# Optimization experiments

Hardware: AMD Instinct MI355X
Metric: run time of the kernel (lower is better)

The kernel has to match this reference:

```python
import jax, jax.numpy as jnp
import numpy as np
from jax import lax

E = 20          # num experts / classes
BN_EPS = 1e-5


def _conv(x, w, b=None):
    # NCHW conv, stride 1, 'same' padding (kernel 3x3 or 1x1)
    y = lax.conv_general_dilated(x, w, (1, 1), 'SAME',
                                 dimension_numbers=('NCHW', 'OIHW', 'NCHW'))
    return y if b is None else y + b[None, :, None, None]


def _lrelu(x):
    return jnp.where(x >= 0, x, 0.2 * x)


def _bn(x, g, b, m, v):
    # inference-mode batchnorm
    scale = g * lax.rsqrt(v + BN_EPS)
    return x * scale[None, :, None, None] + (b - m * scale)[None, :, None, None]


def setup_inputs() -> dict:
    key = jax.random.key(0)
    ks = iter(jax.random.split(key, 40))
    def w(shape):
        return jax.random.normal(next(ks), shape, jnp.float32) * 0.05
    d = {}
    d['x'] = jax.random.normal(next(ks), (2, 3, 192, 192), jnp.float32)
    d['noise'] = jax.random.normal(next(ks), (2, 128, 192, 192), jnp.float32)
    # classification head
    d['cls_w1'] = w((64, 3, 3, 3));    d['cls_b1'] = jnp.zeros((64,), jnp.float32)
    d['cls_w2'] = w((128, 64, 3, 3));  d['cls_b2'] = jnp.zeros((128,), jnp.float32)
    d['cls_w3'] = w((256, 128, 3, 3)); d['cls_b3'] = jnp.zeros((256,), jnp.float32)
    d['cls_w4'] = w((512, 256, 1, 1)); d['cls_b4'] = jnp.zeros((512,), jnp.float32)
    d['cls_w5'] = w((E, 512, 1, 1));   d['cls_b5'] = jnp.zeros((E,), jnp.float32)
    for c, i in ((128, 1), (256, 2), (512, 3)):
        d[f'bn{i}_g'] = jnp.ones((c,), jnp.float32)
        d[f'bn{i}_b'] = jnp.zeros((c,), jnp.float32)
        d[f'bn{i}_m'] = jnp.zeros((c,), jnp.float32)
        d[f'bn{i}_v'] = jnp.ones((c,), jnp.float32)
    # 20 expert encoders (stacked on leading axis)
    d['enc_w1'] = w((E, 32, 3, 3, 3));    d['enc_b1'] = jnp.zeros((E, 32), jnp.float32)
    d['enc_w2'] = w((E, 64, 32, 3, 3));   d['enc_b2'] = jnp.zeros((E, 64), jnp.float32)
    d['enc_w3'] = w((E, 128, 64, 3, 3));  d['enc_b3'] = jnp.zeros((E, 128), jnp.float32)
    d['enc_w4'] = w((E, 128, 128, 3, 3)); d['enc_b4'] = jnp.zeros((E, 128), jnp.float32)
    # decoder (legacy=False: first two 1x1 convs have no bias)
    d['dec_w1'] = w((64, 128, 1, 1))
    d['dec_w2'] = w((32, 64, 1, 1))
    d['dec_w3'] = w((3, 32, 1, 1)); d['dec_b3'] = jnp.zeros((3,), jnp.float32)
    return d


def reference(x, noise,
              cls_w1, cls_b1, cls_w2, cls_b2, cls_w3, cls_b3,
              cls_w4, cls_b4, cls_w5, cls_b5,
              bn1_g, bn1_b, bn1_m, bn1_v,
              bn2_g, bn2_b, bn2_m, bn2_v,
              bn3_g, bn3_b, bn3_m, bn3_v,
              enc_w1, enc_b1, enc_w2, enc_b2, enc_w3, enc_b3, enc_w4, enc_b4,
              dec_w1, dec_w2, dec_w3, dec_b3):
    B, _, H, W = x.shape
    C = enc_w4.shape[1]  # 128
    # --- classification / routing ---
    h = _lrelu(_conv(x, cls_w1, cls_b1))
    h = _lrelu(_bn(_conv(h, cls_w2, cls_b2), bn1_g, bn1_b, bn1_m, bn1_v))
    h = _lrelu(_bn(_conv(h, cls_w3, cls_b3), bn2_g, bn2_b, bn2_m, bn2_v))
    h = _lrelu(_bn(_conv(h, cls_w4, cls_b4), bn3_g, bn3_b, bn3_m, bn3_v))
    classes = jax.nn.softmax(_conv(h, cls_w5, cls_b5), axis=1)  # [B,E,H,W]
    idx = jnp.argmax(classes, axis=1)  # [B,H,W] top-1 expert per pixel

    # --- run all 20 dense encoders (faithful to original torch.where masking) ---
    def enc(w1, b1, w2, b2, w3, b3, w4, b4):
        e = _lrelu(_conv(x, w1, b1))
        e = _lrelu(_conv(e, w2, b2))
        e = _lrelu(_conv(e, w3, b3))
        return _conv(e, w4, b4)
    embs = jax.vmap(enc)(enc_w1, enc_b1, enc_w2, enc_b2,
                         enc_w3, enc_b3, enc_w4, enc_b4)  # [E,B,128,H,W]
    embs = jnp.moveaxis(embs, 0, 1)  # [B,E,128,H,W]
    sel_idx = jnp.broadcast_to(idx[:, None, None, :, :], (B, 1, C, H, W))
    emb = jnp.take_along_axis(embs, sel_idx, axis=1)[:, 0]  # [B,128,H,W]

    # --- decode with additive noise ---
    d = _conv(emb + noise, dec_w1)
    d = _conv(d, dec_w2)
    out = _conv(d, dec_w3, dec_b3)  # [B,3,H,W]

    # --- load balancing loss ---
    one_hot = jax.nn.one_hot(idx, E, dtype=jnp.float32)          # [B,H,W,E]
    density = one_hot.reshape(B, -1, E).mean(axis=1)             # [B,E]
    density_proxy = classes.reshape(B, E, -1).mean(axis=-1)      # [B,E]
    lb = (density_proxy * density).mean() * float(E * E)
    return out, lb * 0.1
```

## Files before the change

kernel.cpp:

```cpp
#include <hip/hip_runtime.h>
#include <hip/hip_bf16.h>

typedef __hip_bfloat16 bf16;
typedef unsigned short u16;
typedef short s16x8 __attribute__((ext_vector_type(8)));
typedef float f32x4 __attribute__((ext_vector_type(4)));
#define MFMA16(a, b, c) __builtin_amdgcn_mfma_f32_16x16x32_bf16(a, b, c, 0, 0, 0)

#define HW_   36864
#define WP_   194
#define HWP_  37636
#define W_    192
#define SP_   9216

__device__ __forceinline__ float ldin(const void* p, size_t i, int f32) {
    return f32 ? ((const float*)p)[i] : __bfloat162float(((const bf16*)p)[i]);
}
__device__ __forceinline__ int probe_f32(const void* pr) {
    return ((const unsigned*)pr)[0] == 0x3F800000u;
}
__device__ __forceinline__ u16 f2bf(float f) {
    bf16 h = __float2bfloat16(f);
    return *reinterpret_cast<u16*>(&h);
}

__global__ __launch_bounds__(256) void pad_x_k(const void* __restrict__ x,
                                               float* __restrict__ xpad,
                                               const void* __restrict__ pr) {
    const int f32 = probe_f32(pr);
    int i = blockIdx.x * 256 + threadIdx.x;
    if (i >= 2 * 3 * HW_) return;
    int w = i % W_;
    int h = (i / W_) % W_;
    int c = i / HW_;
    xpad[(size_t)c * HWP_ + (size_t)(h + 1) * WP_ + (w + 1)] = ldin(x, i, f32);
}

__global__ __launch_bounds__(256) void conv3x3_k(
    const float* __restrict__ in, const void* __restrict__ wgt,
    const void* __restrict__ bias, const void* __restrict__ bng,
    const void* __restrict__ bnb, const void* __restrict__ bnm,
    const void* __restrict__ bnv, float* __restrict__ out,
    int Cin, int Cout, int lrelu, const void* __restrict__ pr)
{
    extern __shared__ float wl[];
    const int f32 = probe_f32(pr);
    const int tid = threadIdx.x;
    const int co0 = blockIdx.y * 8;
    const int b   = blockIdx.z;
    const int n = Cin * 72;
    for (int i = tid; i < n; i += 256) {
        int u = i & 7, r = i >> 3;
        int ci = r / 9, tap = r - ci * 9;
        wl[i] = ldin(wgt, ((size_t)(co0 + u) * Cin + ci) * 9 + tap, f32);
    }
    __syncthreads();

    const int pixb = blockIdx.x * 1024 + tid;
    int off[4];
#pragma unroll
    for (int p = 0; p < 4; ++p) {
        int pix = pixb + p * 256;
        int h = pix / W_, w = pix - h * W_;
        off[p] = (h + 1) * WP_ + (w + 1);
    }
    float acc[32];
#pragma unroll
    for (int i = 0; i < 32; ++i) acc[i] = 0.f;

    const int doff[9] = {-(WP_+1), -WP_, -(WP_-1), -1, 0, 1, WP_-1, WP_, WP_+1};
    const float* inb = in + (size_t)b * Cin * HWP_;
    for (int ci = 0; ci < Cin; ++ci) {
        const float* ip = inb + (size_t)ci * HWP_;
        const float* wp = wl + ci * 72;
#pragma unroll
        for (int tap = 0; tap < 9; ++tap) {
            const float4 wa = *(const float4*)(wp + tap * 8);
            const float4 wb = *(const float4*)(wp + tap * 8 + 4);
            const int d = doff[tap];
            float v[4];
#pragma unroll
            for (int p = 0; p < 4; ++p) v[p] = ip[off[p] + d];
#pragma unroll
            for (int p = 0; p < 4; ++p) {
                acc[p*8+0] += v[p] * wa.x;  acc[p*8+1] += v[p] * wa.y;
                acc[p*8+2] += v[p] * wa.z;  acc[p*8+3] += v[p] * wa.w;
                acc[p*8+4] += v[p] * wb.x;  acc[p*8+5] += v[p] * wb.y;
                acc[p*8+6] += v[p] * wb.z;  acc[p*8+7] += v[p] * wb.w;
            }
        }
    }

#pragma unroll
    for (int u = 0; u < 8; ++u) {
        const int co = co0 + u;
        float s = 1.f, t = 0.f;
        if (bng) {
            float g = ldin(bng, co, f32), bb = ldin(bnb, co, f32);
            float m = ldin(bnm, co, f32), vv = ldin(bnv, co, f32);
            s = g * rsqrtf(vv + 1e-5f);
            t = bb - m * s;
        }
        const float bs = bias ? ldin(bias, co, f32) : 0.f;
        float* op = out + ((size_t)b * Cout + co) * HWP_;
#pragma unroll
        for (int p = 0; p < 4; ++p) {
            float val = (acc[p*8+u] + bs) * s + t;
            if (lrelu) val = val >= 0.f ? val : 0.2f * val;
            op[off[p]] = val;
        }
    }
}

__global__ __launch_bounds__(256) void conv1x1s_k(
    const float* __restrict__ in, const void* __restrict__ wgt,
    const void* __restrict__ bias, const void* __restrict__ bng,
    const void* __restrict__ bnb, const void* __restrict__ bnm,
    const void* __restrict__ bnv, float* __restrict__ out,
    int Cin, int pix0, const void* __restrict__ pr)
{
    extern __shared__ float wl[];
    const int f32 = probe_f32(pr);
    const int tid = threadIdx.x;
    const int co0 = blockIdx.y * 8;
    const int b   = blockIdx.z;
    const int n = Cin * 8;
    for (int i = tid; i < n; i += 256) {
        int u = i & 7, ci = i >> 3;
        wl[i] = ldin(wgt, (size_t)(co0 + u) * Cin + ci, f32);
    }
    __syncthreads();

    const int pixb = pix0 + blockIdx.x * 1024 + tid;
    int off[4], lp[4];
#pragma unroll
    for (int p = 0; p < 4; ++p) {
        int pix = pixb + p * 256;
        lp[p] = pix - pix0;
        int h = pix / W_, w = pix - h * W_;
        off[p] = (h + 1) * WP_ + (w + 1);
    }
    float acc[32];
#pragma unroll
    for (int i = 0; i < 32; ++i) acc[i] = 0.f;

    for (int ci = 0; ci < Cin; ++ci) {
        const float* ip = in + ((size_t)b * Cin + ci) * HWP_;
        const float4 wa = *(const float4*)(wl + ci * 8);
        const float4 wb = *(const float4*)(wl + ci * 8 + 4);
        float v[4];
#pragma unroll
        for (int p = 0; p < 4; ++p) v[p] = ip[off[p]];
#pragma unroll
        for (int p = 0; p < 4; ++p) {
            acc[p*8+0] += v[p] * wa.x;  acc[p*8+1] += v[p] * wa.y;
            acc[p*8+2] += v[p] * wa.z;  acc[p*8+3] += v[p] * wa.w;
            acc[p*8+4] += v[p] * wb.x;  acc[p*8+5] += v[p] * wb.y;
            acc[p*8+6] += v[p] * wb.z;  acc[p*8+7] += v[p] * wb.w;
        }
    }

#pragma unroll
    for (int u = 0; u < 8; ++u) {
        const int co = co0 + u;
        float g = ldin(bng, co, f32), bb = ldin(bnb, co, f32);
        float m = ldin(bnm, co, f32), vv = ldin(bnv, co, f32);
        float s = g * rsqrtf(vv + 1e-5f);
        float t = bb - m * s;
        const float bs = ldin(bias, co, f32);
        float* op = out + ((size_t)b * 512 + co) * SP_;
#pragma unroll
        for (int p = 0; p < 4; ++p) {
            float val = (acc[p*8+u] + bs) * s + t;
            val = val >= 0.f ? val : 0.2f * val;
            op[lp[p]] = val;
        }
    }
}

__global__ __launch_bounds__(256) void heads_k(
    const float* __restrict__ c4q, const void* __restrict__ w5,
    const void* __restrict__ b5, int* __restrict__ idx,
    float* __restrict__ proxy, float* __restrict__ cntg, int pix0,
    const void* __restrict__ pr)
{
    extern __shared__ float wl[];
    __shared__ float sums[20];
    __shared__ float cnts[20];
    const int f32 = probe_f32(pr);
    const int tid = threadIdx.x;
    const int b = blockIdx.y;
    for (int i = tid; i < 512 * 20; i += 256) {
        int e = i % 20, ci = i / 20;
        wl[ci * 20 + e] = ldin(w5, (size_t)e * 512 + ci, f32);
    }
    if (tid < 20) { sums[tid] = 0.f; cnts[tid] = 0.f; }
    __syncthreads();

    const int lpix = blockIdx.x * 256 + tid;

    float acc[20];
#pragma unroll
    for (int e = 0; e < 20; ++e) acc[e] = ldin(b5, e, f32);
    const float* ip = c4q + (size_t)b * 512 * SP_;
    for (int ci = 0; ci < 512; ++ci) {
        const float v = ip[(size_t)ci * SP_ + lpix];
        const float* wp = wl + ci * 20;
#pragma unroll
        for (int e = 0; e < 20; ++e) acc[e] += v * wp[e];
    }

    float m = acc[0]; int am = 0;
#pragma unroll
    for (int e = 1; e < 20; ++e) if (acc[e] > m) { m = acc[e]; am = e; }
    float prb[20], ssum = 0.f;
#pragma unroll
    for (int e = 0; e < 20; ++e) { prb[e] = expf(acc[e] - m); ssum += prb[e]; }
    const float inv = 1.f / ssum;
    idx[b * HW_ + pix0 + lpix] = am;

    const int lane = tid & 63;
#pragma unroll
    for (int e = 0; e < 20; ++e) {
        float p = prb[e] * inv;
        p += __shfl_down(p, 32); p += __shfl_down(p, 16); p += __shfl_down(p, 8);
        p += __shfl_down(p, 4);  p += __shfl_down(p, 2);  p += __shfl_down(p, 1);
        if (lane == 0) atomicAdd(&sums[e], p);
        unsigned long long bal = __ballot(am == e);
        if (lane == 0) atomicAdd(&cnts[e], (float)__popcll(bal));
    }
    __syncthreads();
    if (tid < 20) {
        atomicAdd(&proxy[b * 20 + tid], sums[tid]);
        atomicAdd(&cntg[b * 20 + tid], cnts[tid]);
    }
}

__global__ __launch_bounds__(256) void wtx_k(const void* __restrict__ w,
                                             u16* __restrict__ wt,
                                             int Cout, int Cin, int nTot,
                                             const void* __restrict__ pr) {
    const int f32 = probe_f32(pr);
    int i = blockIdx.x * 256 + threadIdx.x;
    if (i >= nTot) return;
    int ci = i % Cin; int r = i / Cin;
    int co = r % Cout; r /= Cout;
    int tap = r % 9; int e = r / 9;
    size_t src = ((size_t)(e * Cout + co) * Cin + ci) * 9 + tap;
    wt[i] = f2bf(ldin(w, src, f32));
}

__global__ __launch_bounds__(512) void fused_expert_k(
    const float* __restrict__ xpad, const int* __restrict__ idx,
    const void* __restrict__ ew1, const void* __restrict__ eb1,
    const u16* __restrict__ Wt2, const void* __restrict__ eb2,
    const u16* __restrict__ Wt3, const void* __restrict__ eb3,
    const u16* __restrict__ Wt4, const void* __restrict__ eb4,
    float* __restrict__ emb, const void* __restrict__ pr)
{
    __shared__ __align__(16) char smem_[137216];
    u16*   e2s = (u16*)smem_;
    u16*   e3s = (u16*)(smem_ + 54272);
    u16*   e1s = (u16*)(smem_ + 54272);
    float* xs  = (float*)smem_;
    float* wl1 = (float*)(smem_ + 6912);
    u16*   w2s = (u16*)(smem_ + 86016);
    __shared__ int s_sel[256];
    __shared__ int s_wc[8];

    const int f32 = probe_f32(pr);
    const int tid  = threadIdx.x;
    const int lane = tid & 63, wv = tid >> 6;
    const int ml = lane & 15, q8 = (lane >> 4) * 8, m0 = (lane >> 4) * 4;
    const int b = blockIdx.y;
    const int eid = blockIdx.z;
    const int ty = blockIdx.x / 12, tx = blockIdx.x - ty * 12;
    const int Oh = ty * 16, Ow = tx * 16;

    {
        int sel = 0;
        if (tid < 256) {
            const int r = tid >> 4, c = tid & 15;
            sel = (idx[b * HW_ + (Oh + r) * W_ + (Ow + c)] == eid);
        }
        const unsigned long long m = __ballot(sel);
        if (lane == 0) s_wc[wv] = __popcll(m);
        __syncthreads();
        int cnt = 0;
#pragma unroll
        for (int w = 0; w < 8; ++w) cnt += s_wc[w];
        if (cnt == 0) return;
        int pre = 0;
        for (int w = 0; w < wv; ++w) pre += s_wc[w];
        if (sel)
            s_sel[pre + __popcll(m & ((1ull << lane) - 1ull))] = tid;
    }

    for (int i = tid; i < 24 * 24 * 3; i += 512) {
        int ch = i % 3, pxl = i / 3;
        int r = pxl / 24, c = pxl - r * 24;
        int ir = Oh - 4 + r, ic = Ow - 4 + c;
        float v = 0.f;
        if (ir >= -1 && ir < 193 && ic >= -1 && ic < 193)
            v = xpad[((size_t)b * 3 + ch) * HWP_ + (size_t)(ir + 1) * WP_ + (ic + 1)];
        xs[pxl * 3 + ch] = v;
    }
    for (int i = tid; i < 896; i += 512) {
        if (i < 864) {
            int co = i & 31, k = i >> 5;
            int ci = k / 9, tap = k - ci * 9;
            wl1[i] = ldin(ew1, (size_t)eid * 864 + ((size_t)co * 3 + ci) * 9 + tap, f32);
        } else {
            wl1[i] = ldin(eb1, (size_t)eid * 32 + (i - 864), f32);
        }
    }
    {
        const u16* Wt2e = Wt2 + (size_t)eid * 9 * 64 * 32;
        for (int i = tid; i < 2304; i += 512) {
            int r = i >> 2, part = i & 3;
            *(uint4*)(w2s + (size_t)r * 40 + part * 8) =
                *(const uint4*)(Wt2e + (size_t)r * 32 + part * 8);
        }
    }
    __syncthreads();

    if (tid < 484) {
        const int p = tid;
        const int r1 = p / 22, c1 = p - r1 * 22;
        const int ir = Oh - 3 + r1, ic = Ow - 3 + c1;
        const int inimg = (ir >= 0 && ir < 192 && ic >= 0 && ic < 192);
        float a1[32];
#pragma unroll
        for (int co = 0; co < 32; ++co) a1[co] = 0.f;
        if (inimg) {
#pragma unroll
            for (int ci = 0; ci < 3; ++ci)
#pragma unroll
                for (int tap = 0; tap < 9; ++tap) {
                    const int dy = tap / 3, dx = tap - dy * 3;
                    const float xv = xs[((r1 + dy) * 24 + (c1 + dx)) * 3 + ci];
                    const float* wp = wl1 + (ci * 9 + tap) * 32;
#pragma unroll
                    for (int co = 0; co < 32; ++co) a1[co] += xv * wp[co];
                }
        }
        u16 pk[32];
#pragma unroll
        for (int co = 0; co < 32; ++co) {
            float v = 0.f;
            if (inimg) {
                v = a1[co] + wl1[864 + co];
                v = v >= 0.f ? v : 0.2f * v;
            }
            pk[co] = f2bf(v);
        }
#pragma unroll
        for (int ch = 0; ch < 4; ++ch)
            *(uint4*)(e1s + ((size_t)ch * 488 + p) * 8) = ((const uint4*)pk)[ch];
    }
    __syncthreads();

    {
        int pxv[4], r2v[4], c2v[4];
#pragma unroll
        for (int j = 0; j < 4; ++j) {
            int t = wv + 8 * j; if (t > 24) t = 24;
            int px = t * 16 + ml;
            pxv[j] = px; r2v[j] = px / 20; c2v[j] = px - (px / 20) * 20;
        }
        f32x4 acc2[4][4];
#pragma unroll
        for (int j = 0; j < 4; ++j)
#pragma unroll
            for (int n = 0; n < 4; ++n) acc2[j][n] = (f32x4){0.f,0.f,0.f,0.f};

#pragma unroll
        for (int tap = 0; tap < 9; ++tap) {
            const int dy = tap / 3, dx = tap - dy * 3;
            s16x8 aW[4];
#pragma unroll
            for (int n = 0; n < 4; ++n)
                aW[n] = *(const s16x8*)(w2s + ((size_t)tap * 64 + n * 16 + ml) * 40 + q8);
#pragma unroll
            for (int j = 0; j < 4; ++j) {
                const int lin = (r2v[j] + dy) * 22 + (c2v[j] + dx);
                const s16x8 bA = *(const s16x8*)(e1s + ((size_t)(q8 >> 3) * 488 + lin) * 8);
#pragma unroll
                for (int n = 0; n < 4; ++n) acc2[j][n] = MFMA16(aW[n], bA, acc2[j][n]);
            }
        }
        __syncthreads();
#pragma unroll
        for (int j = 0; j < 4; ++j) {
            const int px = pxv[j];
            const int r2 = r2v[j], c2 = c2v[j];
            const int ir = Oh - 2 + r2, ic = Ow - 2 + c2;
            const int inimg = (ir >= 0 && ir < 192 && ic >= 0 && ic < 192);
#pragma unroll
            for (int n = 0; n < 4; ++n) {
                u16 pk[4];
#pragma unroll
                for (int r = 0; r < 4; ++r) {
                    const int co = n * 16 + m0 + r;
                    float v = 0.f;
                    if (inimg) {
                        v = acc2[j][n][r] + ldin(eb2, (size_t)eid * 64 + co, f32);
                        v = v >= 0.f ? v : 0.2f * v;
                    }
                    pk[r] = f2bf(v);
                }
                const int chunk = (n * 16 + m0) >> 3;
                *(uint2*)(e2s + ((size_t)chunk * 424 + px) * 8 + (m0 & 4)) = *(const uint2*)pk;
            }
        }
    }
    __syncthreads();

    {
        const u16* Wt3e = Wt3 + (size_t)eid * 9 * 128 * 64;
        const int np = wv >> 2;
        const int w4 = wv & 3;
        int pxv[6], r3v[6], c3v[6];
#pragma unroll
        for (int j = 0; j < 6; ++j) {
            int t = w4 + 4 * j; if (t > 20) t = 20;
            int px = t * 16 + ml;
            pxv[j] = px; r3v[j] = px / 18; c3v[j] = px - (px / 18) * 18;
        }
        f32x4 acc3[6][4];
#pragma unroll
        for (int j = 0; j < 6; ++j)
#pragma unroll
            for (int n = 0; n < 4; ++n) acc3[j][n] = (f32x4){0.f,0.f,0.f,0.f};

#pragma unroll
        for (int tap = 0; tap < 9; ++tap) {
            const int dy = tap / 3, dx = tap - dy * 3;
#pragma unroll
            for (int cc = 0; cc < 2; ++cc) {
                s16x8 aW[4];
#pragma unroll
                for (int n = 0; n < 4; ++n) {
                    const int co = np * 64 + n * 16 + ml;
                    aW[n] = *(const s16x8*)(Wt3e + ((size_t)tap * 128 + co) * 64 + cc * 32 + q8);
                }
                const int chunk = cc * 4 + (q8 >> 3);
#pragma unroll
                for (int j = 0; j < 6; ++j) {
                    const int lin = (r3v[j] + dy) * 20 + (c3v[j] + dx);
                    const s16x8 bA = *(const s16x8*)(e2s + ((size_t)chunk * 424 + lin) * 8);
#pragma unroll
                    for (int n = 0; n < 4; ++n) acc3[j][n] = MFMA16(aW[n], bA, acc3[j][n]);
                }
            }
        }
        float b3[4][4];
#pragma unroll
        for (int n = 0; n < 4; ++n)
#pragma unroll
            for (int r = 0; r < 4; ++r)
                b3[n][r] = ldin(eb3, (size_t)eid * 128 + np * 64 + n * 16 + m0 + r, f32);
#pragma unroll
        for (int j = 0; j < 6; ++j) {
            const int px = pxv[j];
            if (px >= 324) continue;
            const int r3 = r3v[j], c3 = c3v[j];
            const int ir = Oh - 1 + r3, ic = Ow - 1 + c3;
            const int inimg = (ir >= 0 && ir < 192 && ic >= 0 && ic < 192);
#pragma unroll
            for (int n = 0; n < 4; ++n) {
                u16 pk[4];
#pragma unroll
                for (int r = 0; r < 4; ++r) {
                    float v = 0.f;
                    if (inimg) {
                        v = acc3[j][n][r] + b3[n][r];
                        v = v >= 0.f ? v : 0.2f * v;
                    }
                    pk[r] = f2bf(v);
                }
                const int chunk = (np * 64 + n * 16 + m0) >> 3;
                *(uint2*)(e3s + ((size_t)chunk * 324 + px) * 8 + (m0 & 4)) = *(const uint2*)pk;
            }
        }
    }
    __syncthreads();

    {
        const u16* Wt4e = Wt4 + (size_t)eid * 9 * 128 * 128;
        int cnt = 0;
#pragma unroll
        for (int w = 0; w < 8; ++w) cnt += s_wc[w];
        const int mtiles = (cnt + 15) >> 4;
        const int n0 = wv * 16;
        float bs[4];
#pragma unroll
        for (int r = 0; r < 4; ++r) bs[r] = ldin(eb4, (size_t)eid * 128 + n0 + m0 + r, f32);
        for (int mt = 0; mt < mtiles; ++mt) {
            const int li = mt * 16 + ml;
            const int lpx = (li < cnt) ? s_sel[li] : 0;
            const int rr = lpx >> 4, cc2 = lpx & 15;
            f32x4 acc = {0.f,0.f,0.f,0.f};
#pragma unroll
            for (int tap = 0; tap < 9; ++tap) {
                const int dy = tap / 3, dx = tap - dy * 3;
                const int lin = (rr + dy) * 18 + (cc2 + dx);
#pragma unroll
                for (int c0 = 0; c0 < 128; c0 += 32) {
                    const s16x8 bA = *(const s16x8*)(e3s + ((size_t)((c0 + q8) >> 3) * 324 + lin) * 8);
                    const s16x8 aW = *(const s16x8*)(Wt4e + ((size_t)tap * 128 + n0 + ml) * 128 + c0 + q8);
                    acc = MFMA16(aW, bA, acc);
                }
            }
            if (li < cnt) {
                const int g = (Oh + rr) * W_ + Ow + cc2;
#pragma unroll
                for (int r = 0; r < 4; ++r)
                    emb[((size_t)b * 128 + n0 + m0 + r) * HW_ + g] = acc[r] + bs[r];
            }
        }
    }
}

__global__ __launch_bounds__(256) void dec_fused_k(
    const float* __restrict__ emb, const void* __restrict__ noise,
    const void* __restrict__ dw1, const void* __restrict__ dw2,
    const void* __restrict__ dw3, const void* __restrict__ db3,
    void* __restrict__ outb, const void* __restrict__ pr)
{
    __shared__ float w1s[128 * 64];
    __shared__ float w2s[64 * 32];
    __shared__ float w3s[100];
    const int f32 = probe_f32(pr);
    const int tid = threadIdx.x;
    for (int i = tid; i < 128 * 64; i += 256) {
        int ci = i >> 6, co = i & 63;
        w1s[i] = ldin(dw1, (size_t)co * 128 + ci, f32);
    }
    for (int i = tid; i < 64 * 32; i += 256) {
        int ci = i >> 5, co = i & 31;
        w2s[i] = ldin(dw2, (size_t)co * 64 + ci, f32);
    }
    if (tid < 96) {
        int ci = tid / 3, k = tid - ci * 3;
        w3s[ci * 3 + k] = ldin(dw3, (size_t)k * 32 + ci, f32);
    }
    if (tid >= 96 && tid < 99) w3s[96 + tid - 96] = ldin(db3, tid - 96, f32);
    __syncthreads();

    const int b = blockIdx.y;
    const int pix = blockIdx.x * 256 + tid;

    float h1[64];
#pragma unroll
    for (int i = 0; i < 64; ++i) h1[i] = 0.f;
    for (int ci = 0; ci < 128; ++ci) {
        const size_t base = ((size_t)b * 128 + ci) * HW_ + pix;
        const float v = emb[base] + ldin(noise, base, f32);
        const float* wp = w1s + ci * 64;
#pragma unroll
        for (int c4 = 0; c4 < 16; ++c4) {
            const float4 w = *(const float4*)(wp + c4 * 4);
            h1[c4*4+0] += v * w.x; h1[c4*4+1] += v * w.y;
            h1[c4*4+2] += v * w.z; h1[c4*4+3] += v * w.w;
        }
    }
    float h2[32];
#pragma unroll
    for (int i = 0; i < 32; ++i) h2[i] = 0.f;
#pragma unroll
    for (int ci = 0; ci < 64; ++ci) {
        const float v = h1[ci];
        const float* wp = w2s + ci * 32;
#pragma unroll
        for (int c4 = 0; c4 < 8; ++c4) {
            const float4 w = *(const float4*)(wp + c4 * 4);
            h2[c4*4+0] += v * w.x; h2[c4*4+1] += v * w.y;
            h2[c4*4+2] += v * w.z; h2[c4*4+3] += v * w.w;
        }
    }
    float a0 = w3s[96], a1 = w3s[97], a2 = w3s[98];
#pragma unroll
    for (int ci = 0; ci < 32; ++ci) {
        const float v = h2[ci];
        a0 += v * w3s[ci * 3 + 0];
        a1 += v * w3s[ci * 3 + 1];
        a2 += v * w3s[ci * 3 + 2];
    }
    const size_t o0 = (size_t)(b * 3 + 0) * HW_ + pix;
    const size_t o1 = (size_t)(b * 3 + 1) * HW_ + pix;
    const size_t o2 = (size_t)(b * 3 + 2) * HW_ + pix;
    if (f32) {
        ((float*)outb)[o0] = a0; ((float*)outb)[o1] = a1; ((float*)outb)[o2] = a2;
    } else {
        ((bf16*)outb)[o0] = __float2bfloat16(a0);
        ((bf16*)outb)[o1] = __float2bfloat16(a1);
        ((bf16*)outb)[o2] = __float2bfloat16(a2);
    }
}

__global__ void lb_k(const float* __restrict__ proxy, const float* __restrict__ cnt,
                     void* __restrict__ out, const void* __restrict__ pr) {
    const int f32 = probe_f32(pr);
    const int t = threadIdx.x;
    const float inv = 1.0f / (float)HW_;
    float v = 0.f;
    if (t < 40) v = (proxy[t] * inv) * (cnt[t] * inv);
#pragma unroll
    for (int o = 32; o > 0; o >>= 1) v += __shfl_down(v, o);
    if (t == 0) {
        if (f32) ((float*)out)[221184] = v;
        else     ((bf16*)out)[221184] = __float2bfloat16(v);
    }
}

extern "C" void kernel_launch(void* const* d_in, const int* in_sizes, int n_in,
                              void* d_out, int out_size, void* d_ws, size_t ws_size,
                              hipStream_t stream) {
    (void)in_sizes; (void)n_in; (void)out_size; (void)ws_size;
    const void* x    = d_in[0];
    const void* noise= d_in[1];
    const void* cw1  = d_in[2];  const void* cb1 = d_in[3];
    const void* cw2  = d_in[4];  const void* cb2 = d_in[5];
    const void* cw3  = d_in[6];  const void* cb3 = d_in[7];
    const void* cw4  = d_in[8];  const void* cb4 = d_in[9];
    const void* cw5  = d_in[10]; const void* cb5 = d_in[11];
    const void* bn1g = d_in[12]; const void* bn1b = d_in[13];
    const void* bn1m = d_in[14]; const void* bn1v = d_in[15];
    const void* bn2g = d_in[16]; const void* bn2b = d_in[17];
    const void* bn2m = d_in[18]; const void* bn2v = d_in[19];
    const void* bn3g = d_in[20]; const void* bn3b = d_in[21];
    const void* bn3m = d_in[22]; const void* bn3v = d_in[23];
    const void* ew1  = d_in[24]; const void* eb1 = d_in[25];
    const void* ew2  = d_in[26]; const void* eb2 = d_in[27];
    const void* ew3  = d_in[28]; const void* eb3 = d_in[29];
    const void* ew4  = d_in[30]; const void* eb4 = d_in[31];
    const void* dw1  = d_in[32];
    const void* dw2  = d_in[33];
    const void* dw3  = d_in[34]; const void* db3 = d_in[35];
    const void* pr   = bn1v;

    char* ws = (char*)d_ws;
    constexpr size_t SZ_XPAD = (((size_t)2*3*HWP_*4) + 255) & ~(size_t)255;
    constexpr size_t O_BUF2  = SZ_XPAD;
    constexpr size_t SZ_BUF2 = (size_t)2*256*HWP_*4;
    constexpr size_t O_BUF1  = O_BUF2 + SZ_BUF2;
    constexpr size_t SZ_BUF1 = (size_t)2*128*HWP_*4;
    constexpr size_t O_IDX   = O_BUF1 + SZ_BUF1;
    constexpr size_t O_STAT  = O_IDX + (size_t)2*HW_*4;
    constexpr size_t WS_USED = O_STAT + 512;

    float* xpad  = (float*)(ws);
    float* buf2  = (float*)(ws + O_BUF2);
    int*   idx   = (int*)  (ws + O_IDX);
    float* proxy = (float*)(ws + O_STAT);
    float* cntg  = proxy + 40;

    float* c1  = buf2;
    float* c3  = buf2;
    float* c2  = (float*)(ws + O_BUF1);
    float* c4q = (float*)(ws + O_BUF1);
    float* emb = buf2;
    u16* Wt2 = (u16*)(ws + O_BUF1);
    u16* Wt3 = Wt2 + 368640;
    u16* Wt4 = Wt3 + 1474560;

    hipMemsetAsync(d_ws, 0, WS_USED, stream);

    dim3 blk(256);
    pad_x_k<<<dim3((2*3*HW_ + 255)/256), blk, 0, stream>>>(x, xpad, pr);

    conv3x3_k<<<dim3(36,  8, 2), blk,   3*288, stream>>>(xpad, cw1, cb1, nullptr,nullptr,nullptr,nullptr, c1,   3,  64, 1, pr);
    conv3x3_k<<<dim3(36, 16, 2), blk,  64*288, stream>>>(c1,   cw2, cb2, bn1g,bn1b,bn1m,bn1v,           c2,  64, 128, 1, pr);
    conv3x3_k<<<dim3(36, 32, 2), blk, 128*288, stream>>>(c2,   cw3, cb3, bn2g,bn2b,bn2m,bn2v,           c3, 128, 256, 1, pr);
    for (int s = 0; s < 4; ++s) {
        conv1x1s_k<<<dim3(9, 64, 2), blk, 256*32, stream>>>(c3, cw4, cb4, bn3g,bn3b,bn3m,bn3v, c4q, 256, s*SP_, pr);
        heads_k<<<dim3(36, 2), blk, 512*20*4, stream>>>(c4q, cw5, cb5, idx, proxy, cntg, s*SP_, pr);
    }

    wtx_k<<<dim3(1440),  blk, 0, stream>>>(ew2, Wt2,  64,  32,  368640, pr);
    wtx_k<<<dim3(5760),  blk, 0, stream>>>(ew3, Wt3, 128,  64, 1474560, pr);
    wtx_k<<<dim3(11520), blk, 0, stream>>>(ew4, Wt4, 128, 128, 2949120, pr);

    fused_expert_k<<<dim3(144, 2, 20), dim3(512), 0, stream>>>(
        xpad, idx, ew1, eb1, Wt2, eb2, Wt3, eb3, Wt4, eb4, emb, pr);

    dec_fused_k<<<dim3(144, 2), blk, 0, stream>>>(emb, noise, dw1, dw2, dw3, db3, d_out, pr);
    lb_k<<<1, 64, 0, stream>>>(proxy, cntg, d_out, pr);
}
```

Measured before the change: 2.507 ms.

## Compact conv3 to pixels needed by selected outputs and software-pipeline weight loads

Builds a compacted list of the 18x18 layer-3 pixels that are actually needed by the selected output pixels (dilated selection mask), and computes conv3 only for those tiles instead of all 324 positions. Conv3 and conv4 weight loads are double-buffered so global weight fetches overlap MFMA work. Conv4 now processes up to four 16-pixel tiles per weight fetch, reusing each weight fragment across more pixels. This adds per-block scan overhead and extra register pressure from the multi-buffered fragments and accumulators.

Result: no change. 2.508 ms (+0.1%).

```diff
diff --git a/kernel.cpp b/kernel.cpp
--- a/kernel.cpp
+++ b/kernel.cpp
@@ -267,6 +267,9 @@
     u16*   w2s = (u16*)(smem_ + 86016);
     __shared__ int s_sel[256];
     __shared__ int s_wc[8];
+    __shared__ unsigned long long s_selq[4];
+    __shared__ u16 s_l3[324];
+    __shared__ int s_c3;
 
     const int f32 = probe_f32(pr);
     const int tid  = threadIdx.x;
@@ -284,7 +287,10 @@
             sel = (idx[b * HW_ + (Oh + r) * W_ + (Ow + c)] == eid);
         }
         const unsigned long long m = __ballot(sel);
-        if (lane == 0) s_wc[wv] = __popcll(m);
+        if (lane == 0) {
+            s_wc[wv] = __popcll(m);
+            if (wv < 4) s_selq[wv] = m;
+        }
         __syncthreads();
         int cnt = 0;
 #pragma unroll
@@ -294,6 +300,36 @@
         for (int w = 0; w < wv; ++w) pre += s_wc[w];
         if (sel)
             s_sel[pre + __popcll(m & ((1ull << lane) - 1ull))] = tid;
+    }
+
+    if (wv == 0) {
+        unsigned need = 0;
+        const int r3 = lane;
+        if (r3 < 18) {
+            unsigned m = 0;
+#pragma unroll
+            for (int d = 0; d < 3; ++d) {
+                const int r = r3 - 2 + d;
+                if (r >= 0 && r < 16)
+                    m |= (unsigned)((s_selq[r >> 2] >> ((r & 3) * 16)) & 0xFFFFull);
+            }
+            need = (m | (m << 1) | (m << 2)) & 0x3FFFFu;
+        }
+        const int pc = __popc(need);
+        int inc = pc;
+#pragma unroll
+        for (int o = 1; o < 32; o <<= 1) {
+            const int t = __shfl_up(inc, o);
+            if (lane >= o) inc += t;
+        }
+        int k = inc - pc;
+        unsigned mm = need;
+        while (mm) {
+            const int c = __ffs(mm) - 1;
+            mm &= mm - 1;
+            s_l3[k++] = (u16)(r3 * 18 + c);
+        }
+        if (lane == 17) s_c3 = inc;
     }
 
     for (int i = tid; i < 24 * 24 * 3; i += 512) {
@@ -420,11 +456,15 @@
         const u16* Wt3e = Wt3 + (size_t)eid * 9 * 128 * 64;
         const int np = wv >> 2;
         const int w4 = wv & 3;
+        const int cnt3 = s_c3;
+        const int tiles3 = (cnt3 + 15) >> 4;
+        const int jc = (w4 < tiles3) ? ((tiles3 - w4 + 3) >> 2) : 0;
         int pxv[6], r3v[6], c3v[6];
 #pragma unroll
         for (int j = 0; j < 6; ++j) {
-            int t = w4 + 4 * j; if (t > 20) t = 20;
-            int px = t * 16 + ml;
+            int li = (w4 + 4 * j) * 16 + ml;
+            if (li >= cnt3) li = cnt3 - 1;
+            const int px = s_l3[li];
             pxv[j] = px; r3v[j] = px / 18; c3v[j] = px - (px / 18) * 18;
         }
         f32x4 acc3[6][4];
@@ -433,27 +473,35 @@
 #pragma unroll
             for (int n = 0; n < 4; ++n) acc3[j][n] = (f32x4){0.f,0.f,0.f,0.f};
 
-#pragma unroll
-        for (int tap = 0; tap < 9; ++tap) {
-            const int dy = tap / 3, dx = tap - dy * 3;
-#pragma unroll
-            for (int cc = 0; cc < 2; ++cc) {
-                s16x8 aW[4];
-#pragma unroll
-                for (int n = 0; n < 4; ++n) {
-                    const int co = np * 64 + n * 16 + ml;
-                    aW[n] = *(const s16x8*)(Wt3e + ((size_t)tap * 128 + co) * 64 + cc * 32 + q8);
-                }
-                const int chunk = cc * 4 + (q8 >> 3);
-#pragma unroll
-                for (int j = 0; j < 6; ++j) {
-                    const int lin = (r3v[j] + dy) * 20 + (c3v[j] + dx);
-                    const s16x8 bA = *(const s16x8*)(e2s + ((size_t)chunk * 424 + lin) * 8);
-#pragma unroll
-                    for (int n = 0; n < 4; ++n) acc3[j][n] = MFMA16(aW[n], bA, acc3[j][n]);
-                }
-            }
-        }
+#define LW3(dst, g) { const int tp_ = (g) >> 1, cc_ = (g) & 1;                         \
+    dst[0] = *(const s16x8*)(Wt3e + ((size_t)tp_*128 + np*64 +  0 + ml)*64 + cc_*32 + q8); \
+    dst[1] = *(const s16x8*)(Wt3e + ((size_t)tp_*128 + np*64 + 16 + ml)*64 + cc_*32 + q8); \
+    dst[2] = *(const s16x8*)(Wt3e + ((size_t)tp_*128 + np*64 + 32 + ml)*64 + cc_*32 + q8); \
+    dst[3] = *(const s16x8*)(Wt3e + ((size_t)tp_*128 + np*64 + 48 + ml)*64 + cc_*32 + q8); }
+#define C3GROUP(BUF, g) { const int tp_ = (g) >> 1, cc_ = (g) & 1;                     \
+    const int dy_ = tp_ / 3, dx_ = tp_ - dy_ * 3;                                      \
+    const int ch_ = cc_ * 4 + (q8 >> 3);                                               \
+    _Pragma("unroll")                                                                  \
+    for (int j = 0; j < 6; ++j) if (j < jc) {                                          \
+        const int lin_ = (r3v[j] + dy_) * 20 + (c3v[j] + dx_);                         \
+        const s16x8 bA_ = *(const s16x8*)(e2s + ((size_t)ch_ * 424 + lin_) * 8);       \
+        acc3[j][0] = MFMA16(BUF[0], bA_, acc3[j][0]);                                  \
+        acc3[j][1] = MFMA16(BUF[1], bA_, acc3[j][1]);                                  \
+        acc3[j][2] = MFMA16(BUF[2], bA_, acc3[j][2]);                                  \
+        acc3[j][3] = MFMA16(BUF[3], bA_, acc3[j][3]); } }
+
+        s16x8 aA[4], aB[4];
+        LW3(aA, 0);
+#pragma unroll
+        for (int g = 0; g < 18; g += 2) {
+            LW3(aB, g + 1);
+            C3GROUP(aA, g);
+            if (g + 2 < 18) LW3(aA, g + 2);
+            C3GROUP(aB, g + 1);
+        }
+#undef LW3
+#undef C3GROUP
+
         float b3[4][4];
 #pragma unroll
         for (int n = 0; n < 4; ++n)
@@ -462,8 +510,8 @@
                 b3[n][r] = ldin(eb3, (size_t)eid * 128 + np * 64 + n * 16 + m0 + r, f32);
 #pragma unroll
         for (int j = 0; j < 6; ++j) {
+            if (j >= jc) continue;
             const int px = pxv[j];
-            if (px >= 324) continue;
             const int r3 = r3v[j], c3 = c3v[j];
             const int ir = Oh - 1 + r3, ic = Ow - 1 + c3;
             const int inimg = (ir >= 0 && ir < 192 && ic >= 0 && ic < 192);
@@ -496,29 +544,57 @@
         float bs[4];
 #pragma unroll
         for (int r = 0; r < 4; ++r) bs[r] = ldin(eb4, (size_t)eid * 128 + n0 + m0 + r, f32);
-        for (int mt = 0; mt < mtiles; ++mt) {
-            const int li = mt * 16 + ml;
-            const int lpx = (li < cnt) ? s_sel[li] : 0;
-            const int rr = lpx >> 4, cc2 = lpx & 15;
-            f32x4 acc = {0.f,0.f,0.f,0.f};
-#pragma unroll
-            for (int tap = 0; tap < 9; ++tap) {
-                const int dy = tap / 3, dx = tap - dy * 3;
-                const int lin = (rr + dy) * 18 + (cc2 + dx);
-#pragma unroll
-                for (int c0 = 0; c0 < 128; c0 += 32) {
-                    const s16x8 bA = *(const s16x8*)(e3s + ((size_t)((c0 + q8) >> 3) * 324 + lin) * 8);
-                    const s16x8 aW = *(const s16x8*)(Wt4e + ((size_t)tap * 128 + n0 + ml) * 128 + c0 + q8);
-                    acc = MFMA16(aW, bA, acc);
+
+#define LW4(dst, g) { const int tp_ = (g) >> 2, c0_ = ((g) & 3) * 32;                  \
+    dst = *(const s16x8*)(Wt4e + ((size_t)tp_ * 128 + n0 + ml) * 128 + c0_ + q8); }
+#define C4GROUP(BUF, g) { const int tp_ = (g) >> 2, cq_ = ((g) & 3) * 32 + q8;         \
+    const int dy_ = tp_ / 3, dx_ = tp_ - dy_ * 3;                                      \
+    const size_t cb_ = (size_t)(cq_ >> 3) * 324;                                       \
+    _Pragma("unroll")                                                                  \
+    for (int u = 0; u < 4; ++u) if (u < mc) {                                          \
+        const int lin_ = (rrv[u] + dy_) * 18 + (ccv[u] + dx_);                         \
+        const s16x8 bA_ = *(const s16x8*)(e3s + (cb_ + lin_) * 8);                     \
+        acc4[u] = MFMA16(BUF, bA_, acc4[u]); } }
+
+        for (int mt0 = 0; mt0 < mtiles; mt0 += 4) {
+            const int mc = (mtiles - mt0 < 4) ? (mtiles - mt0) : 4;
+            int rrv[4], ccv[4], liv[4];
+#pragma unroll
+            for (int u = 0; u < 4; ++u) {
+                const int li = (mt0 + u) * 16 + ml;
+                int lc = li; if (lc >= cnt) lc = cnt - 1;
+                const int lpx = s_sel[lc];
+                liv[u] = li; rrv[u] = lpx >> 4; ccv[u] = lpx & 15;
+            }
+            f32x4 acc4[4];
+#pragma unroll
+            for (int u = 0; u < 4; ++u) acc4[u] = (f32x4){0.f,0.f,0.f,0.f};
+
+            s16x8 wA, wB, wC, wD;
+            LW4(wA, 0); LW4(wB, 1);
+#pragma unroll
+            for (int g = 0; g < 36; g += 4) {
+                LW4(wC, g + 2);
+                LW4(wD, g + 3);
+                C4GROUP(wA, g);
+                C4GROUP(wB, g + 1);
+                if (g + 4 < 36) LW4(wA, g + 4);
+                if (g + 5 < 36) LW4(wB, g + 5);
+                C4GROUP(wC, g + 2);
+                C4GROUP(wD, g + 3);
+            }
+#pragma unroll
+            for (int u = 0; u < 4; ++u) {
+                if (u < mc && liv[u] < cnt) {
+                    const int g2 = (Oh + rrv[u]) * W_ + Ow + ccv[u];
+#pragma unroll
+                    for (int r = 0; r < 4; ++r)
+                        emb[((size_t)b * 128 + n0 + m0 + r) * HW_ + g2] = acc4[u][r] + bs[r];
                 }
             }
-            if (li < cnt) {
-                const int g = (Oh + rr) * W_ + Ow + cc2;
-#pragma unroll
-                for (int r = 0; r < 4; ++r)
-                    emb[((size_t)b * 128 + n0 + m0 + r) * HW_ + g] = acc[r] + bs[r];
-            }
-        }
+        }
+#undef LW4
+#undef C4GROUP
     }
 }
 
```
